# Optimization experiments

Measured on AMD Instinct MI355X. Metric: run time of the kernel, lower is better.

## Reference

```python
import jax, jax.numpy as jnp
import numpy as np

U = 128  # linear_units

def setup_inputs() -> dict:
    key = jax.random.key(0)
    k1, k2, k3, k4, k5, k6 = jax.random.split(key, 6)
    B, S, D = 16, 2048, 128
    x = jax.random.normal(k1, (B, S, D), dtype=jnp.float32)
    t = jax.random.uniform(k2, (B, S), dtype=jnp.float32)
    # glorot_uniform inits
    lim_qk = np.sqrt(6.0 / (D + U)).astype(np.float32)
    Wq = jax.random.uniform(k3, (D, U), minval=-lim_qk, maxval=lim_qk, dtype=jnp.float32)
    Wk = jax.random.uniform(k4, (D, U), minval=-lim_qk, maxval=lim_qk, dtype=jnp.float32)
    lim_s = np.sqrt(6.0 / (1 + S)).astype(np.float32)
    theta = jax.random.uniform(k5, (1, S), minval=-lim_s, maxval=lim_s, dtype=jnp.float32)
    mu = jax.random.uniform(k6, (1, S), minval=-lim_s, maxval=lim_s, dtype=jnp.float32)
    return {"x": x, "t": t, "Wq": Wq, "Wk": Wk, "theta": theta, "mu": mu}

def reference(x, t, Wq, Wk, theta, mu):
    # x: (B,S,D), t: (B,S), theta/mu: (1,S)
    scale = jnp.sqrt(jnp.asarray(U, dtype=x.dtype))
    q = x @ Wq                                   # (B,S,U)
    k = x @ Wk                                   # (B,S,U)
    scores = jnp.einsum('biu,bju->bij', q, k) / scale  # (B,S,S)
    alphas = jax.nn.softmax(scores, axis=-1)
    gn = jnp.einsum('bij,bjd->bid', alphas, x)   # weighted sum == alphas @ x, (B,S,D)
    time_fact = jax.nn.sigmoid(theta - mu * t)   # (B,S)
    v = jnp.sum(gn * time_fact[:, :, None], axis=1)  # (B,D)
    return v
```

## Files before the change

### kernel.cpp

```cpp
#include <hip/hip_runtime.h>
#include <hip/hip_bf16.h>

#define SS 2048
#define DD 128
#define BB 16
#define LDST 136
#define SCT 268

typedef short bf16x8 __attribute__((ext_vector_type(8)));
typedef float f32x4 __attribute__((ext_vector_type(4)));
typedef unsigned short ushort_t;

__device__ __forceinline__ unsigned short f2bf(float f) {
  union { float f; unsigned u; } v; v.f = f;
  unsigned r = v.u + 0x7fffu + ((v.u >> 16) & 1u);
  return (unsigned short)(r >> 16);
}
__device__ __forceinline__ float fexp2(float x) { return __builtin_amdgcn_exp2f(x); }


__global__ __launch_bounds__(256) void wprep(
    const float* __restrict__ Wq, const float* __restrict__ Wk,
    ushort_t* __restrict__ wt_g) {
  int idx = blockIdx.x * 256 + threadIdx.x;
  int r = idx & 16383, uu = r >> 7, d = r & 127;
  if (idx < 16384)
    wt_g[uu * 128 + d] = f2bf(Wq[d * 128 + uu] * 0.1275174346f);
  else
    wt_g[(uu + 128) * 128 + d] = f2bf(Wk[d * 128 + uu]);
}

__global__ __launch_bounds__(256, 2) void qk_gemm(
    const float* __restrict__ x, const ushort_t* __restrict__ wt_g,
    uint4* __restrict__ qF, uint4* __restrict__ kF) {
  __shared__ ushort_t xs[64 * LDST];
  __shared__ ushort_t sc[64 * SCT];
  const int tid = threadIdx.x, wave = tid >> 6, lane = tid & 63;
  const int lq = lane & 15, quad = lane >> 4;
  const int m0 = blockIdx.x * 64;

#pragma unroll
  for (int i = 0; i < 8; ++i) {
    int idx = i * 256 + tid;
    int row = idx >> 5, c4 = (idx & 31) * 4;
    const float4 v = *(const float4*)(x + (size_t)(m0 + row) * DD + c4);
    ushort4 h;
    h.x = f2bf(v.x); h.y = f2bf(v.y); h.z = f2bf(v.z); h.w = f2bf(v.w);
    *(ushort4*)(&xs[row * LDST + c4]) = h;
  }
  bf16x8 wf[4][4];
#pragma unroll
  for (int nt = 0; nt < 4; ++nt)
#pragma unroll
    for (int ks = 0; ks < 4; ++ks)
      wf[nt][ks] = *(const bf16x8*)(wt_g + (wave * 64 + nt * 16 + lq) * 128 + ks * 32 + quad * 8);
  __syncthreads();

  f32x4 acc[4][4];
#pragma unroll
  for (int mt = 0; mt < 4; ++mt)
#pragma unroll
    for (int nt = 0; nt < 4; ++nt) acc[mt][nt] = (f32x4){0.f, 0.f, 0.f, 0.f};
#pragma unroll
  for (int mt = 0; mt < 4; ++mt) {
    bf16x8 af[4];
#pragma unroll
    for (int ks = 0; ks < 4; ++ks)
      af[ks] = *(const bf16x8*)(&xs[(mt * 16 + lq) * LDST + ks * 32 + quad * 8]);
#pragma unroll
    for (int nt = 0; nt < 4; ++nt)
#pragma unroll
      for (int ks = 0; ks < 4; ++ks)
        acc[mt][nt] = __builtin_amdgcn_mfma_f32_16x16x32_bf16(af[ks], wf[nt][ks], acc[mt][nt], 0, 0, 0);
  }
#pragma unroll
  for (int mt = 0; mt < 4; ++mt)
#pragma unroll
    for (int nt = 0; nt < 4; ++nt)
#pragma unroll
      for (int r = 0; r < 4; ++r)
        sc[(mt * 16 + quad * 4 + r) * SCT + wave * 64 + nt * 16 + lq] = f2bf(acc[mt][nt][r]);
  __syncthreads();
#pragma unroll
  for (int i = 0; i < 8; ++i) {
    int c = i * 256 + tid;
    int lane_c = c & 63, ks_c = (c >> 6) & 3, g_c = (c >> 8) & 3, isk = c >> 10;
    int li = lane_c & 15, qd = lane_c >> 4;
    int col = isk * 128 + ks_c * 32 + qd * 8;
    uint4 v = *(const uint4*)(&sc[(g_c * 16 + li) * SCT + col]);
    size_t G = (size_t)blockIdx.x * 4 + g_c;
    uint4* dst = isk ? kF : qF;
    dst[(G * 4 + ks_c) * 64 + lane_c] = v;
  }
}

__global__ __launch_bounds__(256, 2) void attn_fused(
    const uint4* __restrict__ qF, const uint4* __restrict__ kF,
    const float* __restrict__ t, const float* __restrict__ theta,
    const float* __restrict__ mu, float* __restrict__ w) {
  const int b = blockIdx.x >> 5;
  const int ib = blockIdx.x & 31;
  const int i0 = ib * 64;
  const int tid = threadIdx.x, wave = tid >> 6, lane = tid & 63;
  const int lq = lane & 15, quad = lane >> 4;

  __shared__ float rs_lds[4][64];
  __shared__ float c_lds[64];

  const bf16x8* qc = (const bf16x8*)qF;
  const bf16x8* kc = (const bf16x8*)kF;

  bf16x8 af[4][4];
#pragma unroll
  for (int mt = 0; mt < 4; ++mt)
#pragma unroll
    for (int ks = 0; ks < 4; ++ks)
      af[mt][ks] = qc[((size_t)(b * 128 + ib * 4 + mt) * 4 + ks) * 64 + lane];

  bf16x8 cur[2][4], nxt[2][4];
  auto load_tile = [&](bf16x8 (&f)[2][4], int jt) {
#pragma unroll
    for (int nt = 0; nt < 2; ++nt) {
      int gg = jt * 8 + wave * 2 + nt;
#pragma unroll
      for (int ks = 0; ks < 4; ++ks)
        f[nt][ks] = kc[((size_t)(b * 128 + gg) * 4 + ks) * 64 + lane];
    }
  };

  float rowsum[4][4];
#pragma unroll
  for (int mt = 0; mt < 4; ++mt)
#pragma unroll
    for (int r = 0; r < 4; ++r) rowsum[mt][r] = 0.f;

  auto compute_p1 = [&](bf16x8 (&f)[2][4]) {
#pragma unroll
    for (int nt = 0; nt < 2; ++nt) {
      f32x4 acc[4];
#pragma unroll
      for (int mt = 0; mt < 4; ++mt) acc[mt] = (f32x4){0.f, 0.f, 0.f, 0.f};
#pragma unroll
      for (int ks = 0; ks < 4; ++ks)
#pragma unroll
        for (int mt = 0; mt < 4; ++mt)
          acc[mt] = __builtin_amdgcn_mfma_f32_16x16x32_bf16(af[mt][ks], f[nt][ks], acc[mt], 0, 0, 0);
#pragma unroll
      for (int mt = 0; mt < 4; ++mt)
#pragma unroll
        for (int r = 0; r < 4; ++r) rowsum[mt][r] += fexp2(acc[mt][r]);
    }
  };

  load_tile(cur, 0);
  for (int jt = 0; jt < 16; jt += 2) {
    load_tile(nxt, jt + 1);
    compute_p1(cur);
    if (jt + 2 < 16) load_tile(cur, jt + 2);
    compute_p1(nxt);
  }

#pragma unroll
  for (int d2 = 1; d2 <= 8; d2 <<= 1)
#pragma unroll
    for (int mt = 0; mt < 4; ++mt)
#pragma unroll
      for (int r = 0; r < 4; ++r)
        rowsum[mt][r] += __shfl_xor(rowsum[mt][r], d2, 64);
  if (lq == 0) {
#pragma unroll
    for (int mt = 0; mt < 4; ++mt)
#pragma unroll
      for (int r = 0; r < 4; ++r)
        rs_lds[wave][mt * 16 + quad * 4 + r] = rowsum[mt][r];
  }
  __syncthreads();
  if (tid < 64) {
    float l = rs_lds[0][tid] + rs_lds[1][tid] + rs_lds[2][tid] + rs_lds[3][tid];
    int gi = i0 + tid;
    float z = theta[gi] - mu[gi] * t[b * SS + gi];
    float tf = 1.f / (1.f + fexp2(-z * 1.44269504f));
    c_lds[tid] = tf / l;
  }
  __syncthreads();
  float creg[4][4];
#pragma unroll
  for (int mt = 0; mt < 4; ++mt)
#pragma unroll
    for (int r = 0; r < 4; ++r) creg[mt][r] = c_lds[mt * 16 + quad * 4 + r];

  auto compute_p2 = [&](bf16x8 (&f)[2][4], int jt) {
#pragma unroll
    for (int nt = 0; nt < 2; ++nt) {
      f32x4 acc[4];
#pragma unroll
      for (int mt = 0; mt < 4; ++mt) acc[mt] = (f32x4){0.f, 0.f, 0.f, 0.f};
#pragma unroll
      for (int ks = 0; ks < 4; ++ks)
#pragma unroll
        for (int mt = 0; mt < 4; ++mt)
          acc[mt] = __builtin_amdgcn_mfma_f32_16x16x32_bf16(af[mt][ks], f[nt][ks], acc[mt], 0, 0, 0);
      float cs = 0.f;
#pragma unroll
      for (int mt = 0; mt < 4; ++mt)
#pragma unroll
        for (int r = 0; r < 4; ++r) cs = fmaf(creg[mt][r], fexp2(acc[mt][r]), cs);
      cs += __shfl_xor(cs, 16, 64);
      cs += __shfl_xor(cs, 32, 64);
      if (lane < 16)
        atomicAdd(&w[b * SS + (jt * 8 + wave * 2 + nt) * 16 + lane], cs);
    }
  };

  load_tile(cur, 0);
  for (int jt = 0; jt < 16; jt += 2) {
    load_tile(nxt, jt + 1);
    compute_p2(cur, jt);
    if (jt + 2 < 16) load_tile(cur, jt + 2);
    compute_p2(nxt, jt + 1);
  }
}

__global__ __launch_bounds__(256) void finalize(
    const float* __restrict__ x, const float* __restrict__ w,
    float* __restrict__ out) {
  const int b = blockIdx.x >> 5;
  const int j0 = (blockIdx.x & 31) * 64;
  const int tid = threadIdx.x;
  const int d = tid & 127, jo = tid >> 7;
  float acc = 0.f;
  for (int jj = 0; jj < 32; ++jj) {
    int j = j0 + jj * 2 + jo;
    acc = fmaf(w[b * SS + j], x[((size_t)b * SS + j) * DD + d], acc);
  }
  __shared__ float red[256];
  red[tid] = acc;
  __syncthreads();
  if (tid < 128) atomicAdd(&out[b * DD + tid], red[tid] + red[tid + 128]);
}

extern "C" void kernel_launch(void* const* d_in, const int* in_sizes, int n_in,
                              void* d_out, int out_size, void* d_ws, size_t ws_size,
                              hipStream_t stream) {
  const float* x = (const float*)d_in[0];
  const float* t = (const float*)d_in[1];
  const float* Wq = (const float*)d_in[2];
  const float* Wk = (const float*)d_in[3];
  const float* theta = (const float*)d_in[4];
  const float* mu = (const float*)d_in[5];
  float* out = (float*)d_out;

  uint4* qF = (uint4*)d_ws;
  uint4* kF = qF + (size_t)2048 * 4 * 64;
  ushort_t* wt_g = (ushort_t*)(kF + (size_t)2048 * 4 * 64);
  float* w = (float*)(wt_g + 256 * 128);

  hipMemsetAsync(w, 0, (size_t)BB * SS * sizeof(float), stream);
  hipMemsetAsync(d_out, 0, (size_t)BB * DD * sizeof(float), stream);

  wprep<<<dim3(128), dim3(256), 0, stream>>>(Wq, Wk, wt_g);
  qk_gemm<<<dim3(512), dim3(256), 0, stream>>>(x, wt_g, qF, kF);
  attn_fused<<<dim3(512), dim3(256), 0, stream>>>(qF, kF, t, theta, mu, w);
  finalize<<<dim3(512), dim3(256), 0, stream>>>(x, w, out);
}
```

Measured before the change: 127.9 us.

## Split fused attention into two kernels with key-halved grids for more parallelism

The single two-pass attention kernel becomes two kernels. The first computes softmax row sums, splitting the key range in half across blocks and combining partial sums with atomics into a new workspace buffer. The second applies the time factor and accumulates column weights. Grid size doubles to 1024 blocks, occupancy hints rise from 2 to 4 blocks per CU, explicit register double-buffering is dropped, and MFMA sections are wrapped in s_setprio. This trades an extra launch, a memset, more row-sum atomics and reloading Q for better CU utilisation and latency hiding.

```diff
diff --git a/kernel.cpp b/kernel.cpp
--- a/kernel.cpp
+++ b/kernel.cpp
@@ -94,22 +94,16 @@
   }
 }
 
-__global__ __launch_bounds__(256, 2) void attn_fused(
+__global__ __launch_bounds__(256, 4) void attn_p1(
     const uint4* __restrict__ qF, const uint4* __restrict__ kF,
-    const float* __restrict__ t, const float* __restrict__ theta,
-    const float* __restrict__ mu, float* __restrict__ w) {
-  const int b = blockIdx.x >> 5;
-  const int ib = blockIdx.x & 31;
-  const int i0 = ib * 64;
+    float* __restrict__ l) {
+  const int bx = blockIdx.x;
+  const int b = bx >> 6, ib = (bx >> 1) & 31, jh = bx & 1;
   const int tid = threadIdx.x, wave = tid >> 6, lane = tid & 63;
   const int lq = lane & 15, quad = lane >> 4;
-
   __shared__ float rs_lds[4][64];
-  __shared__ float c_lds[64];
 
   const bf16x8* qc = (const bf16x8*)qF;
-  const bf16x8* kc = (const bf16x8*)kF;
-
   bf16x8 af[4][4];
 #pragma unroll
   for (int mt = 0; mt < 4; ++mt)
@@ -117,16 +111,7 @@
     for (int ks = 0; ks < 4; ++ks)
       af[mt][ks] = qc[((size_t)(b * 128 + ib * 4 + mt) * 4 + ks) * 64 + lane];
 
-  bf16x8 cur[2][4], nxt[2][4];
-  auto load_tile = [&](bf16x8 (&f)[2][4], int jt) {
-#pragma unroll
-    for (int nt = 0; nt < 2; ++nt) {
-      int gg = jt * 8 + wave * 2 + nt;
-#pragma unroll
-      for (int ks = 0; ks < 4; ++ks)
-        f[nt][ks] = kc[((size_t)(b * 128 + gg) * 4 + ks) * 64 + lane];
-    }
-  };
+  const bf16x8* kb = (const bf16x8*)kF + (size_t)b * 128 * 4 * 64 + lane;
 
   float rowsum[4][4];
 #pragma unroll
@@ -134,30 +119,27 @@
 #pragma unroll
     for (int r = 0; r < 4; ++r) rowsum[mt][r] = 0.f;
 
-  auto compute_p1 = [&](bf16x8 (&f)[2][4]) {
-#pragma unroll
-    for (int nt = 0; nt < 2; ++nt) {
-      f32x4 acc[4];
-#pragma unroll
-      for (int mt = 0; mt < 4; ++mt) acc[mt] = (f32x4){0.f, 0.f, 0.f, 0.f};
-#pragma unroll
-      for (int ks = 0; ks < 4; ++ks)
-#pragma unroll
-        for (int mt = 0; mt < 4; ++mt)
-          acc[mt] = __builtin_amdgcn_mfma_f32_16x16x32_bf16(af[mt][ks], f[nt][ks], acc[mt], 0, 0, 0);
+  const f32x4 z4 = {0.f, 0.f, 0.f, 0.f};
+  for (int it = 0; it < 16; ++it) {
+    int g = jh * 64 + it * 4 + wave;
+    bf16x8 f[4];
+#pragma unroll
+    for (int ks = 0; ks < 4; ++ks) f[ks] = kb[((size_t)g * 4 + ks) * 64];
+    f32x4 a[4];
+    __builtin_amdgcn_s_setprio(1);
+#pragma unroll
+    for (int mt = 0; mt < 4; ++mt)
+      a[mt] = __builtin_amdgcn_mfma_f32_16x16x32_bf16(af[mt][0], f[0], z4, 0, 0, 0);
+#pragma unroll
+    for (int ks = 1; ks < 4; ++ks)
 #pragma unroll
       for (int mt = 0; mt < 4; ++mt)
-#pragma unroll
-        for (int r = 0; r < 4; ++r) rowsum[mt][r] += fexp2(acc[mt][r]);
-    }
-  };
-
-  load_tile(cur, 0);
-  for (int jt = 0; jt < 16; jt += 2) {
-    load_tile(nxt, jt + 1);
-    compute_p1(cur);
-    if (jt + 2 < 16) load_tile(cur, jt + 2);
-    compute_p1(nxt);
+        a[mt] = __builtin_amdgcn_mfma_f32_16x16x32_bf16(af[mt][ks], f[ks], a[mt], 0, 0, 0);
+    __builtin_amdgcn_s_setprio(0);
+#pragma unroll
+    for (int mt = 0; mt < 4; ++mt)
+#pragma unroll
+      for (int r = 0; r < 4; ++r) rowsum[mt][r] += fexp2(a[mt][r]);
   }
 
 #pragma unroll
@@ -176,48 +158,71 @@
   }
   __syncthreads();
   if (tid < 64) {
-    float l = rs_lds[0][tid] + rs_lds[1][tid] + rs_lds[2][tid] + rs_lds[3][tid];
-    int gi = i0 + tid;
+    float p = rs_lds[0][tid] + rs_lds[1][tid] + rs_lds[2][tid] + rs_lds[3][tid];
+    atomicAdd(&l[b * SS + ib * 64 + tid], p);
+  }
+}
+
+__global__ __launch_bounds__(256, 4) void attn_p2(
+    const uint4* __restrict__ qF, const uint4* __restrict__ kF,
+    const float* __restrict__ t, const float* __restrict__ theta,
+    const float* __restrict__ mu, const float* __restrict__ l,
+    float* __restrict__ w) {
+  const int bx = blockIdx.x;
+  const int b = bx >> 6, ib = (bx >> 1) & 31, jh = bx & 1;
+  const int tid = threadIdx.x, wave = tid >> 6, lane = tid & 63;
+  const int lq = lane & 15, quad = lane >> 4;
+  __shared__ float c_lds[64];
+
+  if (tid < 64) {
+    int gi = ib * 64 + tid;
     float z = theta[gi] - mu[gi] * t[b * SS + gi];
     float tf = 1.f / (1.f + fexp2(-z * 1.44269504f));
-    c_lds[tid] = tf / l;
-  }
-  __syncthreads();
+    c_lds[tid] = tf / l[b * SS + gi];
+  }
+  __syncthreads();
+
+  const bf16x8* qc = (const bf16x8*)qF;
+  bf16x8 af[4][4];
+#pragma unroll
+  for (int mt = 0; mt < 4; ++mt)
+#pragma unroll
+    for (int ks = 0; ks < 4; ++ks)
+      af[mt][ks] = qc[((size_t)(b * 128 + ib * 4 + mt) * 4 + ks) * 64 + lane];
+
   float creg[4][4];
 #pragma unroll
   for (int mt = 0; mt < 4; ++mt)
 #pragma unroll
     for (int r = 0; r < 4; ++r) creg[mt][r] = c_lds[mt * 16 + quad * 4 + r];
 
-  auto compute_p2 = [&](bf16x8 (&f)[2][4], int jt) {
-#pragma unroll
-    for (int nt = 0; nt < 2; ++nt) {
-      f32x4 acc[4];
-#pragma unroll
-      for (int mt = 0; mt < 4; ++mt) acc[mt] = (f32x4){0.f, 0.f, 0.f, 0.f};
-#pragma unroll
-      for (int ks = 0; ks < 4; ++ks)
-#pragma unroll
-        for (int mt = 0; mt < 4; ++mt)
-          acc[mt] = __builtin_amdgcn_mfma_f32_16x16x32_bf16(af[mt][ks], f[nt][ks], acc[mt], 0, 0, 0);
-      float cs = 0.f;
+  const bf16x8* kb = (const bf16x8*)kF + (size_t)b * 128 * 4 * 64 + lane;
+  const f32x4 z4 = {0.f, 0.f, 0.f, 0.f};
+
+  for (int it = 0; it < 16; ++it) {
+    int g = jh * 64 + it * 4 + wave;
+    bf16x8 f[4];
+#pragma unroll
+    for (int ks = 0; ks < 4; ++ks) f[ks] = kb[((size_t)g * 4 + ks) * 64];
+    f32x4 a[4];
+    __builtin_amdgcn_s_setprio(1);
+#pragma unroll
+    for (int mt = 0; mt < 4; ++mt)
+      a[mt] = __builtin_amdgcn_mfma_f32_16x16x32_bf16(af[mt][0], f[0], z4, 0, 0, 0);
+#pragma unroll
+    for (int ks = 1; ks < 4; ++ks)
 #pragma unroll
       for (int mt = 0; mt < 4; ++mt)
-#pragma unroll
-        for (int r = 0; r < 4; ++r) cs = fmaf(creg[mt][r], fexp2(acc[mt][r]), cs);
-      cs += __shfl_xor(cs, 16, 64);
-      cs += __shfl_xor(cs, 32, 64);
-      if (lane < 16)
-        atomicAdd(&w[b * SS + (jt * 8 + wave * 2 + nt) * 16 + lane], cs);
-    }
-  };
-
-  load_tile(cur, 0);
-  for (int jt = 0; jt < 16; jt += 2) {
-    load_tile(nxt, jt + 1);
-    compute_p2(cur, jt);
-    if (jt + 2 < 16) load_tile(cur, jt + 2);
-    compute_p2(nxt, jt + 1);
+        a[mt] = __builtin_amdgcn_mfma_f32_16x16x32_bf16(af[mt][ks], f[ks], a[mt], 0, 0, 0);
+    __builtin_amdgcn_s_setprio(0);
+    float cs = 0.f;
+#pragma unroll
+    for (int mt = 0; mt < 4; ++mt)
+#pragma unroll
+      for (int r = 0; r < 4; ++r) cs = fmaf(creg[mt][r], fexp2(a[mt][r]), cs);
+    cs += __shfl_xor(cs, 16, 64);
+    cs += __shfl_xor(cs, 32, 64);
+    if (lane < 16) atomicAdd(&w[b * SS + g * 16 + lane], cs);
   }
 }
 
@@ -254,12 +259,15 @@
   uint4* kF = qF + (size_t)2048 * 4 * 64;
   ushort_t* wt_g = (ushort_t*)(kF + (size_t)2048 * 4 * 64);
   float* w = (float*)(wt_g + 256 * 128);
+  float* l = w + (size_t)BB * SS;
 
   hipMemsetAsync(w, 0, (size_t)BB * SS * sizeof(float), stream);
+  hipMemsetAsync(l, 0, (size_t)BB * SS * sizeof(float), stream);
   hipMemsetAsync(d_out, 0, (size_t)BB * DD * sizeof(float), stream);
 
   wprep<<<dim3(128), dim3(256), 0, stream>>>(Wq, Wk, wt_g);
   qk_gemm<<<dim3(512), dim3(256), 0, stream>>>(x, wt_g, qF, kF);
-  attn_fused<<<dim3(512), dim3(256), 0, stream>>>(qF, kF, t, theta, mu, w);
+  attn_p1<<<dim3(1024), dim3(256), 0, stream>>>(qF, kF, l);
+  attn_p2<<<dim3(1024), dim3(256), 0, stream>>>(qF, kF, t, theta, mu, l, w);
   finalize<<<dim3(512), dim3(256), 0, stream>>>(x, w, out);
 }
```

Measured after the change: 131.9 us. 1.03x slower.
